# Optimization experiments

Measured on AMD Instinct MI355X. Metric: run time of the kernel, lower is better.

Reference implementation:

```python
import jax, jax.numpy as jnp
import numpy as np

B, D_IMG, D_NUM, P = 16384, 2048, 256, 128

def setup_inputs() -> dict:
    key = jax.random.key(0)
    ks = jax.random.split(key, 12)
    s = lambda d: 1.0 / np.sqrt(d)
    return {
        "img_feat": jax.random.normal(ks[0], (B, D_IMG), jnp.float32),
        "num_feat": jax.random.normal(ks[1], (B, D_NUM), jnp.float32),
        "Wi1": jax.random.uniform(ks[2], (D_IMG, P), jnp.float32, -s(D_IMG), s(D_IMG)),
        "bi1": jax.random.uniform(ks[3], (P,), jnp.float32, -s(D_IMG), s(D_IMG)),
        "Wi2": jax.random.uniform(ks[4], (P, P), jnp.float32, -s(P), s(P)),
        "bi2": jax.random.uniform(ks[5], (P,), jnp.float32, -s(P), s(P)),
        "Wn1": jax.random.uniform(ks[6], (D_NUM, P), jnp.float32, -s(D_NUM), s(D_NUM)),
        "bn1": jax.random.uniform(ks[7], (P,), jnp.float32, -s(D_NUM), s(D_NUM)),
        "Wn2": jax.random.uniform(ks[8], (P, P), jnp.float32, -s(P), s(P)),
        "bn2": jax.random.uniform(ks[9], (P,), jnp.float32, -s(P), s(P)),
        "log_temp": jnp.asarray(np.log(0.1), jnp.float32),
    }

def _mlp(x, W1, b1, W2, b2):
    h = jax.nn.relu(x @ W1 + b1)
    return h @ W2 + b2

def _l2norm(x, eps=1e-12):
    # matches F.normalize(dim=1): x / max(||x||, eps)
    n = jnp.sqrt(jnp.sum(x * x, axis=1, keepdims=True))
    return x / jnp.maximum(n, eps)

def reference(img_feat, num_feat, Wi1, bi1, Wi2, bi2, Wn1, bn1, Wn2, bn2, log_temp):
    temp = jnp.exp(log_temp)
    ip = _l2norm(_mlp(img_feat, Wi1, bi1, Wi2, bi2))  # [B, P]
    npj = _l2norm(_mlp(num_feat, Wn1, bn1, Wn2, bn2))  # [B, P]
    logits = (ip @ npj.T) / temp                        # [B, B]
    # symmetric cross-entropy with labels = arange(B): targets on the diagonal
    lse_rows = jax.nn.logsumexp(logits, axis=1)  # i2n
    lse_cols = jax.nn.logsumexp(logits, axis=0)  # n2i (logits.T rows)
    diag = jnp.diagonal(logits)
    loss_i2n = jnp.mean(lse_rows - diag)
    loss_n2i = jnp.mean(lse_cols - diag)
    return (loss_i2n + loss_n2i) * 0.5
```

## Files before the change

### kernel.cpp

```cpp
#include <hip/hip_runtime.h>
#include <hip/hip_bf16.h>

typedef __bf16 bf16_t;
typedef __bf16 bf16x8 __attribute__((ext_vector_type(8)));
typedef __bf16 bf16x4 __attribute__((ext_vector_type(4)));
typedef float f32x4 __attribute__((ext_vector_type(4)));

#define NB 16384
#define PP 128
#define NSPLIT 16
#define CG (NB / NSPLIT)
#define BNT 64
#define NT (CG / BNT)

__device__ inline bf16x8 ld8(const bf16_t* p) { return *(const bf16x8*)p; }

__device__ inline void gload_lds16(const bf16_t* g, bf16_t* l) {
  __builtin_amdgcn_global_load_lds(
      (const __attribute__((address_space(1))) unsigned int*)g,
      (__attribute__((address_space(3))) unsigned int*)l, 16, 0, 0);
}

__global__ void transpose_all(const float* __restrict__ Wi1, const float* __restrict__ Wn1,
                              const float* __restrict__ Wi2, const float* __restrict__ Wn2,
                              bf16_t* __restrict__ Wi1t, bf16_t* __restrict__ Wn1t,
                              bf16_t* __restrict__ Wi2t, bf16_t* __restrict__ Wn2t) {
  int idx = blockIdx.x * 256 + threadIdx.x;
  if (idx < 2048 * 128) { int k = idx >> 7, n = idx & 127; Wi1t[n * 2048 + k] = (bf16_t)Wi1[idx]; return; }
  idx -= 2048 * 128;
  if (idx < 256 * 128)  { int k = idx >> 7, n = idx & 127; Wn1t[n * 256 + k]  = (bf16_t)Wn1[idx]; return; }
  idx -= 256 * 128;
  if (idx < 128 * 128)  { int k = idx >> 7, n = idx & 127; Wi2t[n * 128 + k]  = (bf16_t)Wi2[idx]; return; }
  idx -= 128 * 128;
  if (idx < 128 * 128)  { int k = idx >> 7, n = idx & 127; Wn2t[n * 128 + k]  = (bf16_t)Wn2[idx]; }
}

__global__ __launch_bounds__(256, 4) void mlp1_combined(
    const float* __restrict__ Ximg, const float* __restrict__ Xnum,
    const bf16_t* __restrict__ Wit, const bf16_t* __restrict__ Wnt,
    const float* __restrict__ bi, const float* __restrict__ bn,
    bf16_t* __restrict__ Himg, bf16_t* __restrict__ Hnum) {
  __shared__ bf16_t As[32 * 128];
  __shared__ bf16_t Bs[128 * 128];
  const int bid = blockIdx.x;
  const bool isnum = bid >= 512;
  const float* X = isnum ? Xnum : Ximg;
  const bf16_t* Wt = isnum ? Wnt : Wit;
  const float* bias = isnum ? bn : bi;
  bf16_t* H = isnum ? Hnum : Himg;
  const int K = isnum ? 256 : 2048;
  const int t = threadIdx.x, l = t & 63, wid = t >> 6;
  const int wm = wid >> 1, wn = wid & 1;
  const int row0 = (bid & 511) * 32;

  f32x4 acc[4];
#pragma unroll
  for (int j = 0; j < 4; j++) acc[j] = (f32x4){0.f, 0.f, 0.f, 0.f};

  for (int k0 = 0; k0 < K; k0 += 128) {
    __syncthreads();
#pragma unroll
    for (int i = 0; i < 4; i++) {
      int s = t + i * 256;
      int r = s >> 5, c4 = s & 31;
      const float4 f = *(const float4*)(X + (size_t)(row0 + r) * K + k0 + c4 * 4);
      bf16x4 pk;
      pk[0] = (bf16_t)f.x; pk[1] = (bf16_t)f.y; pk[2] = (bf16_t)f.z; pk[3] = (bf16_t)f.w;
      int chunk = c4 >> 1, half = c4 & 1;
      *(bf16x4*)(As + r * 128 + ((chunk ^ (r & 7)) << 3) + half * 4) = pk;
    }
#pragma unroll
    for (int i = 0; i < 8; i++) {
      int s = t + i * 256;
      int r = s >> 4, c = s & 15;
      bf16x8 v = ld8(Wt + (size_t)r * K + k0 + c * 8);
      *(bf16x8*)(Bs + r * 128 + ((c ^ (r & 7)) << 3)) = v;
    }
    __syncthreads();
#pragma unroll
    for (int ks = 0; ks < 4; ks++) {
      int r = wm * 16 + (l & 15);
      int c = ks * 4 + (l >> 4);
      bf16x8 a = ld8(As + r * 128 + ((c ^ (r & 7)) << 3));
#pragma unroll
      for (int nt = 0; nt < 4; nt++) {
        int rb = wn * 64 + nt * 16 + (l & 15);
        bf16x8 b = ld8(Bs + rb * 128 + ((c ^ (rb & 7)) << 3));
        acc[nt] = __builtin_amdgcn_mfma_f32_16x16x32_bf16(a, b, acc[nt], 0, 0, 0);
      }
    }
  }
  int rbase = row0 + wm * 16 + ((l >> 4) << 2);
#pragma unroll
  for (int nt = 0; nt < 4; nt++) {
    int col = wn * 64 + nt * 16 + (l & 15);
    float bv = bias[col];
#pragma unroll
    for (int r4 = 0; r4 < 4; r4++) {
      float v = acc[nt][r4] + bv;
      H[(size_t)(rbase + r4) * PP + col] = (bf16_t)fmaxf(v, 0.f);
    }
  }
}

__global__ __launch_bounds__(256, 3) void mlp2_combined(
    const bf16_t* __restrict__ Himg, const bf16_t* __restrict__ Hnum,
    const bf16_t* __restrict__ Wi2t, const bf16_t* __restrict__ Wn2t,
    const float* __restrict__ bi2, const float* __restrict__ bn2,
    bf16_t* __restrict__ OutI, bf16_t* __restrict__ OutN) {
  __shared__ bf16_t As[32 * 128];
  __shared__ bf16_t Bs[128 * 128];
  __shared__ float rnorm[32];
  const int bid = blockIdx.x;
  const bool isnum = bid >= 512;
  const bf16_t* Hin = isnum ? Hnum : Himg;
  const bf16_t* W2t = isnum ? Wn2t : Wi2t;
  const float* bias = isnum ? bn2 : bi2;
  bf16_t* Out = isnum ? OutN : OutI;
  const int t = threadIdx.x, l = t & 63, wid = t >> 6;
  const int wm = wid >> 1, wn = wid & 1;
  const int row0 = (bid & 511) * 32;
  if (t < 32) rnorm[t] = 0.f;
#pragma unroll
  for (int i = 0; i < 2; i++) {
    int s = t + i * 256;
    int r = s >> 4, c = s & 15;
    bf16x8 v = ld8(Hin + (size_t)(row0 + r) * 128 + c * 8);
    *(bf16x8*)(As + r * 128 + ((c ^ (r & 7)) << 3)) = v;
  }
#pragma unroll
  for (int i = 0; i < 8; i++) {
    int s = t + i * 256;
    int r = s >> 4, c = s & 15;
    bf16x8 v = ld8(W2t + (size_t)r * 128 + c * 8);
    *(bf16x8*)(Bs + r * 128 + ((c ^ (r & 7)) << 3)) = v;
  }
  __syncthreads();
  f32x4 acc[4];
#pragma unroll
  for (int j = 0; j < 4; j++) acc[j] = (f32x4){0.f, 0.f, 0.f, 0.f};
#pragma unroll
  for (int ks = 0; ks < 4; ks++) {
    int r = wm * 16 + (l & 15);
    int c = ks * 4 + (l >> 4);
    bf16x8 a = ld8(As + r * 128 + ((c ^ (r & 7)) << 3));
#pragma unroll
    for (int nt = 0; nt < 4; nt++) {
      int rb = wn * 64 + nt * 16 + (l & 15);
      bf16x8 b = ld8(Bs + rb * 128 + ((c ^ (rb & 7)) << 3));
      acc[nt] = __builtin_amdgcn_mfma_f32_16x16x32_bf16(a, b, acc[nt], 0, 0, 0);
    }
  }
  float vv[4][4];
#pragma unroll
  for (int nt = 0; nt < 4; nt++) {
    int col = wn * 64 + nt * 16 + (l & 15);
    float bv = bias[col];
#pragma unroll
    for (int r4 = 0; r4 < 4; r4++) vv[nt][r4] = acc[nt][r4] + bv;
  }
#pragma unroll
  for (int r4 = 0; r4 < 4; r4++) {
    float p = 0.f;
#pragma unroll
    for (int nt = 0; nt < 4; nt++) p += vv[nt][r4] * vv[nt][r4];
    p += __shfl_xor(p, 1); p += __shfl_xor(p, 2);
    p += __shfl_xor(p, 4); p += __shfl_xor(p, 8);
    if ((l & 15) == 0) atomicAdd(&rnorm[wm * 16 + ((l >> 4) << 2) + r4], p);
  }
  __syncthreads();
#pragma unroll
  for (int r4 = 0; r4 < 4; r4++) {
    int rl = wm * 16 + ((l >> 4) << 2) + r4;
    float sc = 1.f / fmaxf(sqrtf(rnorm[rl]), 1e-12f);
#pragma unroll
    for (int nt = 0; nt < 4; nt++) {
      int col = wn * 64 + nt * 16 + (l & 15);
      int swcol = (((col >> 3) ^ (rl & 7)) << 3) | (col & 7);
      Out[(size_t)(row0 + rl) * 128 + swcol] = (bf16_t)(vv[nt][r4] * sc);
    }
  }
}

__global__ __launch_bounds__(256, 3) void logits_split(
    const bf16_t* __restrict__ IP, const bf16_t* __restrict__ NP,
    const float* __restrict__ log_temp, float* __restrict__ rowpart,
    float* __restrict__ colpart, float* __restrict__ diag) {
  __shared__ bf16_t BsAll[2 * BNT * 128];
  __shared__ float colred[2][CG];
  __shared__ float rowred[2][128];
  int bid = blockIdx.x;
  int sw = (bid & 7) * (128 * NSPLIT / 8) + (bid >> 3);
  int bm = sw >> 4, g = sw & (NSPLIT - 1);
  const int t = threadIdx.x, l = t & 63, wid = t >> 6;
  const int wm = wid >> 1, wn = wid & 1;
  const float invt = __expf(-log_temp[0]);
  const float kk = invt * 1.44269504088896f;

#pragma unroll
  for (int i = 0; i < 8; i++) {
    int s = t + i * 256;
    gload_lds16(IP + (size_t)bm * (128 * 128) + s * 8, BsAll + s * 8);
  }
  __syncthreads();
  bf16x8 af[4][4];
#pragma unroll
  for (int mt = 0; mt < 4; mt++) {
    int r = wm * 64 + mt * 16 + (l & 15);
#pragma unroll
    for (int ks = 0; ks < 4; ks++) {
      int c = ks * 4 + (l >> 4);
      af[mt][ks] = ld8(BsAll + r * 128 + ((c ^ (r & 7)) << 3));
    }
  }
  __syncthreads();
#pragma unroll
  for (int i = 0; i < 4; i++) {
    int s = t + i * 256;
    gload_lds16(NP + (size_t)(g * CG) * 128 + s * 8, BsAll + s * 8);
  }
  __syncthreads();

  f32x4 racc[4];
#pragma unroll
  for (int a = 0; a < 4; a++) racc[a] = (f32x4){0.f, 0.f, 0.f, 0.f};

#pragma unroll 1
  for (int tl = 0; tl < NT; tl++) {
    bf16_t* Bsc = BsAll + (tl & 1) * (BNT * 128);
    if (tl + 1 < NT) {
      bf16_t* Bsn = BsAll + ((tl + 1) & 1) * (BNT * 128);
      const bf16_t* src = NP + (size_t)(g * CG + (tl + 1) * BNT) * 128;
#pragma unroll
      for (int i = 0; i < 4; i++) {
        int s = t + i * 256;
        gload_lds16(src + s * 8, Bsn + s * 8);
      }
    }
    f32x4 acc[4][2];
#pragma unroll
    for (int i = 0; i < 4; i++)
#pragma unroll
      for (int j = 0; j < 2; j++) acc[i][j] = (f32x4){0.f, 0.f, 0.f, 0.f};
#pragma unroll
    for (int ks = 0; ks < 4; ks++) {
      int c = ks * 4 + (l >> 4);
      bf16x8 b[2];
#pragma unroll
      for (int nt = 0; nt < 2; nt++) {
        int rb = wn * 32 + nt * 16 + (l & 15);
        b[nt] = ld8(Bsc + rb * 128 + ((c ^ (rb & 7)) << 3));
      }
#pragma unroll
      for (int mt = 0; mt < 4; mt++) {
        acc[mt][0] = __builtin_amdgcn_mfma_f32_16x16x32_bf16(af[mt][ks], b[0], acc[mt][0], 0, 0, 0);
        acc[mt][1] = __builtin_amdgcn_mfma_f32_16x16x32_bf16(af[mt][ks], b[1], acc[mt][1], 0, 0, 0);
      }
    }
    const int colbase = g * CG + tl * BNT;
    if ((colbase >> 7) == bm) {
#pragma unroll
      for (int mt = 0; mt < 4; mt++)
#pragma unroll
        for (int nt = 0; nt < 2; nt++)
#pragma unroll
          for (int r4 = 0; r4 < 4; r4++) {
            int gr = bm * 128 + wm * 64 + mt * 16 + ((l >> 4) << 2) + r4;
            int gc = colbase + wn * 32 + nt * 16 + (l & 15);
            if (gr == gc) diag[gr] = acc[mt][nt][r4] * invt;
          }
    }
#pragma unroll
    for (int mt = 0; mt < 4; mt++)
#pragma unroll
      for (int nt = 0; nt < 2; nt++) {
        f32x4 y = acc[mt][nt] * kk - kk;
#pragma unroll
        for (int r4 = 0; r4 < 4; r4++) acc[mt][nt][r4] = __builtin_amdgcn_exp2f(y[r4]);
      }
#pragma unroll
    for (int mt = 0; mt < 4; mt++) racc[mt] += acc[mt][0] + acc[mt][1];
#pragma unroll
    for (int nt = 0; nt < 2; nt++) {
      f32x4 cv = (acc[0][nt] + acc[1][nt]) + (acc[2][nt] + acc[3][nt]);
      float cs = (cv[0] + cv[1]) + (cv[2] + cv[3]);
      cs += __shfl_xor(cs, 16); cs += __shfl_xor(cs, 32);
      if (l < 16) colred[wm][tl * BNT + wn * 32 + nt * 16 + l] = cs;
    }
    __syncthreads();
  }
#pragma unroll
  for (int mt = 0; mt < 4; mt++)
#pragma unroll
    for (int r4 = 0; r4 < 4; r4++) {
      float rs = racc[mt][r4];
      rs += __shfl_xor(rs, 1); rs += __shfl_xor(rs, 2);
      rs += __shfl_xor(rs, 4); rs += __shfl_xor(rs, 8);
      if ((l & 15) == 0)
        rowred[wn][wm * 64 + mt * 16 + ((l >> 4) << 2) + r4] = rs;
    }
  __syncthreads();
  if (t < 128)
    rowpart[(size_t)g * NB + bm * 128 + t] = rowred[0][t] + rowred[1][t];
  for (int c = t; c < CG; c += 256)
    colpart[(size_t)bm * NB + g * CG + c] = colred[0][c] + colred[1][c];
}

__global__ void finalize1(const float* __restrict__ rowpart, const float* __restrict__ colpart,
                          const float* __restrict__ diag, float* __restrict__ lossacc) {
  int i = blockIdx.x * 64 + threadIdx.x;
  float rsum = 0.f, csum = 0.f;
#pragma unroll
  for (int g = 0; g < NSPLIT; g++) rsum += rowpart[(size_t)g * NB + i];
#pragma unroll 16
  for (int b = 0; b < 128; b++) csum += colpart[(size_t)b * NB + i];
  float v = 0.5f * (logf(rsum) + logf(csum)) - diag[i];
  for (int m = 1; m < 64; m <<= 1) v += __shfl_xor(v, m);
  if (threadIdx.x == 0) atomicAdd(lossacc, v);
}

__global__ void finalize2(const float* __restrict__ lossacc,
                          const float* __restrict__ log_temp, float* __restrict__ out) {
  out[0] = lossacc[0] / (float)NB + __expf(-log_temp[0]);
}

extern "C" void kernel_launch(void* const* d_in, const int* in_sizes, int n_in,
                              void* d_out, int out_size, void* d_ws, size_t ws_size,
                              hipStream_t stream) {
  const float* img = (const float*)d_in[0];
  const float* num = (const float*)d_in[1];
  const float* Wi1 = (const float*)d_in[2];
  const float* bi1 = (const float*)d_in[3];
  const float* Wi2 = (const float*)d_in[4];
  const float* bi2 = (const float*)d_in[5];
  const float* Wn1 = (const float*)d_in[6];
  const float* bn1 = (const float*)d_in[7];
  const float* Wn2 = (const float*)d_in[8];
  const float* bn2 = (const float*)d_in[9];
  const float* log_temp = (const float*)d_in[10];
  float* out = (float*)d_out;

  char* w = (char*)d_ws;
  bf16_t* ipb   = (bf16_t*)(w);
  bf16_t* npb   = (bf16_t*)(w + (4u << 20));
  bf16_t* h_img = (bf16_t*)(w + (8u << 20));
  bf16_t* h_num = (bf16_t*)(w + (12u << 20));
  float*  colpart = (float*)(w + (8u << 20));
  bf16_t* Wi1t  = (bf16_t*)(w + (16u << 20));
  bf16_t* Wn1t  = (bf16_t*)(w + (16u << 20) + (512u << 10));
  bf16_t* Wi2t  = (bf16_t*)(w + (16u << 20) + (576u << 10));
  bf16_t* Wn2t  = (bf16_t*)(w + (16u << 20) + (640u << 10));
  float*  rowpart = (float*)(w + (16u << 20));
  float*  diag  = (float*)(w + (17u << 20));
  float*  lossacc = (float*)(w + (17u << 20) + (64u << 10));

  hipMemsetAsync(lossacc, 0, sizeof(float), stream);

  transpose_all<<<dim3(1280), 256, 0, stream>>>(Wi1, Wn1, Wi2, Wn2, Wi1t, Wn1t, Wi2t, Wn2t);

  mlp1_combined<<<dim3(1024), 256, 0, stream>>>(img, num, Wi1t, Wn1t, bi1, bn1, h_img, h_num);
  mlp2_combined<<<dim3(1024), 256, 0, stream>>>(h_img, h_num, Wi2t, Wn2t, bi2, bn2, ipb, npb);

  logits_split<<<dim3(128 * NSPLIT), 256, 0, stream>>>(ipb, npb, log_temp, rowpart, colpart, diag);
  finalize1<<<dim3(NB / 64), 64, 0, stream>>>(rowpart, colpart, diag, lossacc);
  finalize2<<<dim3(1), 1, 0, stream>>>(lossacc, log_temp, out);
}
```

Measured before the change: 335.1 us.

## Fuse MLP layers, pre-convert inputs to bf16, widen logits blocks, merge finalize

Fuses the two MLP layers into one kernel so the hidden activations stay in LDS instead of going through global memory. When the workspace is large enough, a prep kernel first converts the inputs to swizzled bf16, and the MLP then loads them with direct global-to-LDS copies. The logits kernel moves to 512-thread blocks with fewer row tiles per wave and accumulates column sums with LDS atomics. The two finalize kernels and the memset are merged using a last-block counter. The input pre-conversion adds a full extra pass over the 128MB image input, and the 512-thread blocks change occupancy and register pressure.

```diff
diff --git a/kernel.cpp b/kernel.cpp
--- a/kernel.cpp
+++ b/kernel.cpp
@@ -3,11 +3,9 @@
 
 typedef __bf16 bf16_t;
 typedef __bf16 bf16x8 __attribute__((ext_vector_type(8)));
-typedef __bf16 bf16x4 __attribute__((ext_vector_type(4)));
 typedef float f32x4 __attribute__((ext_vector_type(4)));
 
 #define NB 16384
-#define PP 128
 #define NSPLIT 16
 #define CG (NB / NSPLIT)
 #define BNT 64
@@ -21,124 +19,156 @@
       (__attribute__((address_space(3))) unsigned int*)l, 16, 0, 0);
 }
 
-__global__ void transpose_all(const float* __restrict__ Wi1, const float* __restrict__ Wn1,
-                              const float* __restrict__ Wi2, const float* __restrict__ Wn2,
-                              bf16_t* __restrict__ Wi1t, bf16_t* __restrict__ Wn1t,
-                              bf16_t* __restrict__ Wi2t, bf16_t* __restrict__ Wn2t) {
-  int idx = blockIdx.x * 256 + threadIdx.x;
-  if (idx < 2048 * 128) { int k = idx >> 7, n = idx & 127; Wi1t[n * 2048 + k] = (bf16_t)Wi1[idx]; return; }
-  idx -= 2048 * 128;
-  if (idx < 256 * 128)  { int k = idx >> 7, n = idx & 127; Wn1t[n * 256 + k]  = (bf16_t)Wn1[idx]; return; }
-  idx -= 256 * 128;
-  if (idx < 128 * 128)  { int k = idx >> 7, n = idx & 127; Wi2t[n * 128 + k]  = (bf16_t)Wi2[idx]; return; }
-  idx -= 128 * 128;
-  if (idx < 128 * 128)  { int k = idx >> 7, n = idx & 127; Wn2t[n * 128 + k]  = (bf16_t)Wn2[idx]; }
-}
-
-__global__ __launch_bounds__(256, 4) void mlp1_combined(
-    const float* __restrict__ Ximg, const float* __restrict__ Xnum,
-    const bf16_t* __restrict__ Wit, const bf16_t* __restrict__ Wnt,
-    const float* __restrict__ bi, const float* __restrict__ bn,
-    bf16_t* __restrict__ Himg, bf16_t* __restrict__ Hnum) {
-  __shared__ bf16_t As[32 * 128];
-  __shared__ bf16_t Bs[128 * 128];
-  const int bid = blockIdx.x;
-  const bool isnum = bid >= 512;
-  const float* X = isnum ? Xnum : Ximg;
-  const bf16_t* Wt = isnum ? Wnt : Wit;
-  const float* bias = isnum ? bn : bi;
-  bf16_t* H = isnum ? Hnum : Himg;
-  const int K = isnum ? 256 : 2048;
-  const int t = threadIdx.x, l = t & 63, wid = t >> 6;
-  const int wm = wid >> 1, wn = wid & 1;
-  const int row0 = (bid & 511) * 32;
-
-  f32x4 acc[4];
-#pragma unroll
-  for (int j = 0; j < 4; j++) acc[j] = (f32x4){0.f, 0.f, 0.f, 0.f};
-
-  for (int k0 = 0; k0 < K; k0 += 128) {
-    __syncthreads();
+__global__ void prep(const float* __restrict__ img, const float* __restrict__ num,
+                     const float* __restrict__ Wi1, const float* __restrict__ Wn1,
+                     const float* __restrict__ Wi2, const float* __restrict__ Wn2,
+                     bf16_t* __restrict__ imgb, bf16_t* __restrict__ numb,
+                     bf16_t* __restrict__ Wi1t, bf16_t* __restrict__ Wn1t,
+                     bf16_t* __restrict__ Wi2t, bf16_t* __restrict__ Wn2t,
+                     float* __restrict__ lossacc, int nimg, int nnum) {
+  int b = blockIdx.x;
+  if (b < nimg) {
+    int base = b * 8192;
 #pragma unroll
     for (int i = 0; i < 4; i++) {
-      int s = t + i * 256;
-      int r = s >> 5, c4 = s & 31;
-      const float4 f = *(const float4*)(X + (size_t)(row0 + r) * K + k0 + c4 * 4);
-      bf16x4 pk;
-      pk[0] = (bf16_t)f.x; pk[1] = (bf16_t)f.y; pk[2] = (bf16_t)f.z; pk[3] = (bf16_t)f.w;
-      int chunk = c4 >> 1, half = c4 & 1;
-      *(bf16x4*)(As + r * 128 + ((chunk ^ (r & 7)) << 3) + half * 4) = pk;
-    }
-#pragma unroll
-    for (int i = 0; i < 8; i++) {
-      int s = t + i * 256;
-      int r = s >> 4, c = s & 15;
-      bf16x8 v = ld8(Wt + (size_t)r * K + k0 + c * 8);
-      *(bf16x8*)(Bs + r * 128 + ((c ^ (r & 7)) << 3)) = v;
-    }
-    __syncthreads();
-#pragma unroll
-    for (int ks = 0; ks < 4; ks++) {
-      int r = wm * 16 + (l & 15);
-      int c = ks * 4 + (l >> 4);
-      bf16x8 a = ld8(As + r * 128 + ((c ^ (r & 7)) << 3));
-#pragma unroll
-      for (int nt = 0; nt < 4; nt++) {
-        int rb = wn * 64 + nt * 16 + (l & 15);
-        bf16x8 b = ld8(Bs + rb * 128 + ((c ^ (rb & 7)) << 3));
-        acc[nt] = __builtin_amdgcn_mfma_f32_16x16x32_bf16(a, b, acc[nt], 0, 0, 0);
-      }
-    }
-  }
-  int rbase = row0 + wm * 16 + ((l >> 4) << 2);
-#pragma unroll
-  for (int nt = 0; nt < 4; nt++) {
-    int col = wn * 64 + nt * 16 + (l & 15);
-    float bv = bias[col];
-#pragma unroll
-    for (int r4 = 0; r4 < 4; r4++) {
-      float v = acc[nt][r4] + bv;
-      H[(size_t)(rbase + r4) * PP + col] = (bf16_t)fmaxf(v, 0.f);
-    }
-  }
-}
-
-__global__ __launch_bounds__(256, 3) void mlp2_combined(
-    const bf16_t* __restrict__ Himg, const bf16_t* __restrict__ Hnum,
+      int e = base + (threadIdx.x + i * 256) * 8;
+      int row = e >> 11, k = e & 2047;
+      float4 f0 = *(const float4*)(img + e);
+      float4 f1 = *(const float4*)(img + e + 4);
+      bf16x8 v;
+      v[0]=(bf16_t)f0.x; v[1]=(bf16_t)f0.y; v[2]=(bf16_t)f0.z; v[3]=(bf16_t)f0.w;
+      v[4]=(bf16_t)f1.x; v[5]=(bf16_t)f1.y; v[6]=(bf16_t)f1.z; v[7]=(bf16_t)f1.w;
+      *(bf16x8*)(imgb + (size_t)row * 2048 + (k ^ ((row & 7) << 3))) = v;
+    }
+    return;
+  }
+  b -= nimg;
+  if (b < nnum) {
+    int base = b * 8192;
+#pragma unroll
+    for (int i = 0; i < 4; i++) {
+      int e = base + (threadIdx.x + i * 256) * 8;
+      int row = e >> 8, k = e & 255;
+      float4 f0 = *(const float4*)(num + e);
+      float4 f1 = *(const float4*)(num + e + 4);
+      bf16x8 v;
+      v[0]=(bf16_t)f0.x; v[1]=(bf16_t)f0.y; v[2]=(bf16_t)f0.z; v[3]=(bf16_t)f0.w;
+      v[4]=(bf16_t)f1.x; v[5]=(bf16_t)f1.y; v[6]=(bf16_t)f1.z; v[7]=(bf16_t)f1.w;
+      *(bf16x8*)(numb + (size_t)row * 256 + (k ^ ((row & 7) << 3))) = v;
+    }
+    return;
+  }
+  b -= nnum;
+  if (b < 1280) {
+    int idx = b * 256 + threadIdx.x;
+    if (idx < 262144) { int k = idx >> 7, n = idx & 127;
+      Wi1t[n * 2048 + (k ^ ((n & 7) << 3))] = (bf16_t)Wi1[idx]; return; }
+    idx -= 262144;
+    if (idx < 32768) { int k = idx >> 7, n = idx & 127;
+      Wn1t[n * 256 + (k ^ ((n & 7) << 3))] = (bf16_t)Wn1[idx]; return; }
+    idx -= 32768;
+    if (idx < 16384) { int k = idx >> 7, n = idx & 127;
+      Wi2t[n * 128 + (k ^ ((n & 7) << 3))] = (bf16_t)Wi2[idx]; return; }
+    idx -= 16384;
+    { int k = idx >> 7, n = idx & 127;
+      Wn2t[n * 128 + (k ^ ((n & 7) << 3))] = (bf16_t)Wn2[idx]; }
+  } else {
+    if (threadIdx.x < 2) lossacc[threadIdx.x] = 0.f;
+  }
+}
+
+template <bool PRE>
+__global__ __launch_bounds__(256, 4) void mlp_fused(
+    const bf16_t* __restrict__ imgb, const bf16_t* __restrict__ numb,
+    const float* __restrict__ imgf, const float* __restrict__ numf,
+    const bf16_t* __restrict__ Wi1t, const bf16_t* __restrict__ Wn1t,
     const bf16_t* __restrict__ Wi2t, const bf16_t* __restrict__ Wn2t,
+    const float* __restrict__ bi1, const float* __restrict__ bn1,
     const float* __restrict__ bi2, const float* __restrict__ bn2,
-    bf16_t* __restrict__ OutI, bf16_t* __restrict__ OutN) {
+    bf16_t* __restrict__ ipb, bf16_t* __restrict__ npb) {
   __shared__ bf16_t As[32 * 128];
   __shared__ bf16_t Bs[128 * 128];
   __shared__ float rnorm[32];
   const int bid = blockIdx.x;
   const bool isnum = bid >= 512;
-  const bf16_t* Hin = isnum ? Hnum : Himg;
-  const bf16_t* W2t = isnum ? Wn2t : Wi2t;
-  const float* bias = isnum ? bn2 : bi2;
-  bf16_t* Out = isnum ? OutN : OutI;
+  const bf16_t* Xb = isnum ? numb : imgb;
+  const float*  Xf = isnum ? numf : imgf;
+  const bf16_t* W1 = isnum ? Wn1t : Wi1t;
+  const bf16_t* W2 = isnum ? Wn2t : Wi2t;
+  const float* b1  = isnum ? bn1 : bi1;
+  const float* b2  = isnum ? bn2 : bi2;
+  bf16_t* Out = isnum ? npb : ipb;
+  const int K = isnum ? 256 : 2048;
   const int t = threadIdx.x, l = t & 63, wid = t >> 6;
   const int wm = wid >> 1, wn = wid & 1;
   const int row0 = (bid & 511) * 32;
   if (t < 32) rnorm[t] = 0.f;
-#pragma unroll
-  for (int i = 0; i < 2; i++) {
-    int s = t + i * 256;
-    int r = s >> 4, c = s & 15;
-    bf16x8 v = ld8(Hin + (size_t)(row0 + r) * 128 + c * 8);
-    *(bf16x8*)(As + r * 128 + ((c ^ (r & 7)) << 3)) = v;
+
+  f32x4 acc[4];
+#pragma unroll
+  for (int j = 0; j < 4; j++) acc[j] = (f32x4){0.f, 0.f, 0.f, 0.f};
+
+  for (int k0 = 0; k0 < K; k0 += 128) {
+    __syncthreads();
+#pragma unroll
+    for (int i = 0; i < 2; i++) {
+      int s = t + i * 256;
+      if constexpr (PRE) {
+        gload_lds16(Xb + (size_t)(row0 + (s >> 4)) * K + k0 + (s & 15) * 8, As + s * 8);
+      } else {
+        int r = s >> 4, c = s & 15;
+        const float* src = Xf + (size_t)(row0 + r) * K + k0 + c * 8;
+        float4 f0 = *(const float4*)(src);
+        float4 f1 = *(const float4*)(src + 4);
+        bf16x8 v;
+        v[0]=(bf16_t)f0.x; v[1]=(bf16_t)f0.y; v[2]=(bf16_t)f0.z; v[3]=(bf16_t)f0.w;
+        v[4]=(bf16_t)f1.x; v[5]=(bf16_t)f1.y; v[6]=(bf16_t)f1.z; v[7]=(bf16_t)f1.w;
+        *(bf16x8*)(As + r * 128 + ((c ^ (r & 7)) << 3)) = v;
+      }
+    }
+#pragma unroll
+    for (int i = 0; i < 8; i++) {
+      int s = t + i * 256;
+      gload_lds16(W1 + (size_t)(s >> 4) * K + k0 + (s & 15) * 8, Bs + s * 8);
+    }
+    __syncthreads();
+#pragma unroll
+    for (int ks = 0; ks < 4; ks++) {
+      int r = wm * 16 + (l & 15);
+      int c = ks * 4 + (l >> 4);
+      bf16x8 a = ld8(As + r * 128 + ((c ^ (r & 7)) << 3));
+#pragma unroll
+      for (int nt = 0; nt < 4; nt++) {
+        int rb = wn * 64 + nt * 16 + (l & 15);
+        bf16x8 bfr = ld8(Bs + rb * 128 + ((c ^ (rb & 7)) << 3));
+        acc[nt] = __builtin_amdgcn_mfma_f32_16x16x32_bf16(a, bfr, acc[nt], 0, 0, 0);
+      }
+    }
+  }
+  __syncthreads();
+  {
+    int rbase = wm * 16 + ((l >> 4) << 2);
+#pragma unroll
+    for (int nt = 0; nt < 4; nt++) {
+      int col = wn * 64 + nt * 16 + (l & 15);
+      float bv = b1[col];
+#pragma unroll
+      for (int r4 = 0; r4 < 4; r4++) {
+        int row = rbase + r4;
+        float h = fmaxf(acc[nt][r4] + bv, 0.f);
+        As[row * 128 + (col ^ ((row & 7) << 3))] = (bf16_t)h;
+      }
+    }
   }
 #pragma unroll
   for (int i = 0; i < 8; i++) {
     int s = t + i * 256;
-    int r = s >> 4, c = s & 15;
-    bf16x8 v = ld8(W2t + (size_t)r * 128 + c * 8);
-    *(bf16x8*)(Bs + r * 128 + ((c ^ (r & 7)) << 3)) = v;
-  }
-  __syncthreads();
-  f32x4 acc[4];
-#pragma unroll
-  for (int j = 0; j < 4; j++) acc[j] = (f32x4){0.f, 0.f, 0.f, 0.f};
+    gload_lds16(W2 + (size_t)(s >> 4) * 128 + (s & 15) * 8, Bs + s * 8);
+  }
+  __syncthreads();
+  f32x4 acc2[4];
+#pragma unroll
+  for (int j = 0; j < 4; j++) acc2[j] = (f32x4){0.f, 0.f, 0.f, 0.f};
 #pragma unroll
   for (int ks = 0; ks < 4; ks++) {
     int r = wm * 16 + (l & 15);
@@ -147,17 +177,17 @@
 #pragma unroll
     for (int nt = 0; nt < 4; nt++) {
       int rb = wn * 64 + nt * 16 + (l & 15);
-      bf16x8 b = ld8(Bs + rb * 128 + ((c ^ (rb & 7)) << 3));
-      acc[nt] = __builtin_amdgcn_mfma_f32_16x16x32_bf16(a, b, acc[nt], 0, 0, 0);
+      bf16x8 bfr = ld8(Bs + rb * 128 + ((c ^ (rb & 7)) << 3));
+      acc2[nt] = __builtin_amdgcn_mfma_f32_16x16x32_bf16(a, bfr, acc2[nt], 0, 0, 0);
     }
   }
   float vv[4][4];
 #pragma unroll
   for (int nt = 0; nt < 4; nt++) {
     int col = wn * 64 + nt * 16 + (l & 15);
-    float bv = bias[col];
-#pragma unroll
-    for (int r4 = 0; r4 < 4; r4++) vv[nt][r4] = acc[nt][r4] + bv;
+    float bv = b2[col];
+#pragma unroll
+    for (int r4 = 0; r4 < 4; r4++) vv[nt][r4] = acc2[nt][r4] + bv;
   }
 #pragma unroll
   for (int r4 = 0; r4 < 4; r4++) {
@@ -176,18 +206,18 @@
 #pragma unroll
     for (int nt = 0; nt < 4; nt++) {
       int col = wn * 64 + nt * 16 + (l & 15);
-      int swcol = (((col >> 3) ^ (rl & 7)) << 3) | (col & 7);
+      int swcol = col ^ ((rl & 7) << 3);
       Out[(size_t)(row0 + rl) * 128 + swcol] = (bf16_t)(vv[nt][r4] * sc);
     }
   }
 }
 
-__global__ __launch_bounds__(256, 3) void logits_split(
+__global__ __launch_bounds__(512, 6) void logits_split(
     const bf16_t* __restrict__ IP, const bf16_t* __restrict__ NP,
     const float* __restrict__ log_temp, float* __restrict__ rowpart,
     float* __restrict__ colpart, float* __restrict__ diag) {
   __shared__ bf16_t BsAll[2 * BNT * 128];
-  __shared__ float colred[2][CG];
+  __shared__ float colred[CG];
   __shared__ float rowred[2][128];
   int bid = blockIdx.x;
   int sw = (bid & 7) * (128 * NSPLIT / 8) + (bid >> 3);
@@ -197,16 +227,17 @@
   const float invt = __expf(-log_temp[0]);
   const float kk = invt * 1.44269504088896f;
 
-#pragma unroll
-  for (int i = 0; i < 8; i++) {
-    int s = t + i * 256;
+  for (int i = t; i < CG; i += 512) colred[i] = 0.f;
+#pragma unroll
+  for (int i = 0; i < 4; i++) {
+    int s = t + i * 512;
     gload_lds16(IP + (size_t)bm * (128 * 128) + s * 8, BsAll + s * 8);
   }
   __syncthreads();
-  bf16x8 af[4][4];
-#pragma unroll
-  for (int mt = 0; mt < 4; mt++) {
-    int r = wm * 64 + mt * 16 + (l & 15);
+  bf16x8 af[2][4];
+#pragma unroll
+  for (int mt = 0; mt < 2; mt++) {
+    int r = wm * 32 + mt * 16 + (l & 15);
 #pragma unroll
     for (int ks = 0; ks < 4; ks++) {
       int c = ks * 4 + (l >> 4);
@@ -215,15 +246,15 @@
   }
   __syncthreads();
 #pragma unroll
-  for (int i = 0; i < 4; i++) {
-    int s = t + i * 256;
+  for (int i = 0; i < 2; i++) {
+    int s = t + i * 512;
     gload_lds16(NP + (size_t)(g * CG) * 128 + s * 8, BsAll + s * 8);
   }
   __syncthreads();
 
-  f32x4 racc[4];
-#pragma unroll
-  for (int a = 0; a < 4; a++) racc[a] = (f32x4){0.f, 0.f, 0.f, 0.f};
+  f32x4 racc[2];
+  racc[0] = (f32x4){0.f, 0.f, 0.f, 0.f};
+  racc[1] = (f32x4){0.f, 0.f, 0.f, 0.f};
 
 #pragma unroll 1
   for (int tl = 0; tl < NT; tl++) {
@@ -232,14 +263,14 @@
       bf16_t* Bsn = BsAll + ((tl + 1) & 1) * (BNT * 128);
       const bf16_t* src = NP + (size_t)(g * CG + (tl + 1) * BNT) * 128;
 #pragma unroll
-      for (int i = 0; i < 4; i++) {
-        int s = t + i * 256;
+      for (int i = 0; i < 2; i++) {
+        int s = t + i * 512;
         gload_lds16(src + s * 8, Bsn + s * 8);
       }
     }
-    f32x4 acc[4][2];
-#pragma unroll
-    for (int i = 0; i < 4; i++)
+    f32x4 acc[2][2];
+#pragma unroll
+    for (int i = 0; i < 2; i++)
 #pragma unroll
       for (int j = 0; j < 2; j++) acc[i][j] = (f32x4){0.f, 0.f, 0.f, 0.f};
 #pragma unroll
@@ -252,7 +283,7 @@
         b[nt] = ld8(Bsc + rb * 128 + ((c ^ (rb & 7)) << 3));
       }
 #pragma unroll
-      for (int mt = 0; mt < 4; mt++) {
+      for (int mt = 0; mt < 2; mt++) {
         acc[mt][0] = __builtin_amdgcn_mfma_f32_16x16x32_bf16(af[mt][ks], b[0], acc[mt][0], 0, 0, 0);
         acc[mt][1] = __builtin_amdgcn_mfma_f32_16x16x32_bf16(af[mt][ks], b[1], acc[mt][1], 0, 0, 0);
       }
@@ -260,18 +291,18 @@
     const int colbase = g * CG + tl * BNT;
     if ((colbase >> 7) == bm) {
 #pragma unroll
-      for (int mt = 0; mt < 4; mt++)
+      for (int mt = 0; mt < 2; mt++)
 #pragma unroll
         for (int nt = 0; nt < 2; nt++)
 #pragma unroll
           for (int r4 = 0; r4 < 4; r4++) {
-            int gr = bm * 128 + wm * 64 + mt * 16 + ((l >> 4) << 2) + r4;
+            int gr = bm * 128 + wm * 32 + mt * 16 + ((l >> 4) << 2) + r4;
             int gc = colbase + wn * 32 + nt * 16 + (l & 15);
             if (gr == gc) diag[gr] = acc[mt][nt][r4] * invt;
           }
     }
 #pragma unroll
-    for (int mt = 0; mt < 4; mt++)
+    for (int mt = 0; mt < 2; mt++)
 #pragma unroll
       for (int nt = 0; nt < 2; nt++) {
         f32x4 y = acc[mt][nt] * kk - kk;
@@ -279,35 +310,36 @@
         for (int r4 = 0; r4 < 4; r4++) acc[mt][nt][r4] = __builtin_amdgcn_exp2f(y[r4]);
       }
 #pragma unroll
-    for (int mt = 0; mt < 4; mt++) racc[mt] += acc[mt][0] + acc[mt][1];
+    for (int mt = 0; mt < 2; mt++) racc[mt] += acc[mt][0] + acc[mt][1];
 #pragma unroll
     for (int nt = 0; nt < 2; nt++) {
-      f32x4 cv = (acc[0][nt] + acc[1][nt]) + (acc[2][nt] + acc[3][nt]);
+      f32x4 cv = acc[0][nt] + acc[1][nt];
       float cs = (cv[0] + cv[1]) + (cv[2] + cv[3]);
       cs += __shfl_xor(cs, 16); cs += __shfl_xor(cs, 32);
-      if (l < 16) colred[wm][tl * BNT + wn * 32 + nt * 16 + l] = cs;
+      if (l < 16) atomicAdd(&colred[tl * BNT + wn * 32 + nt * 16 + l], cs);
     }
     __syncthreads();
   }
 #pragma unroll
-  for (int mt = 0; mt < 4; mt++)
+  for (int mt = 0; mt < 2; mt++)
 #pragma unroll
     for (int r4 = 0; r4 < 4; r4++) {
       float rs = racc[mt][r4];
       rs += __shfl_xor(rs, 1); rs += __shfl_xor(rs, 2);
       rs += __shfl_xor(rs, 4); rs += __shfl_xor(rs, 8);
       if ((l & 15) == 0)
-        rowred[wn][wm * 64 + mt * 16 + ((l >> 4) << 2) + r4] = rs;
+        rowred[wn][wm * 32 + mt * 16 + ((l >> 4) << 2) + r4] = rs;
     }
   __syncthreads();
   if (t < 128)
     rowpart[(size_t)g * NB + bm * 128 + t] = rowred[0][t] + rowred[1][t];
-  for (int c = t; c < CG; c += 256)
-    colpart[(size_t)bm * NB + g * CG + c] = colred[0][c] + colred[1][c];
-}
-
-__global__ void finalize1(const float* __restrict__ rowpart, const float* __restrict__ colpart,
-                          const float* __restrict__ diag, float* __restrict__ lossacc) {
+  for (int c = t; c < CG; c += 512)
+    colpart[(size_t)bm * NB + g * CG + c] = colred[c];
+}
+
+__global__ void finalize(const float* __restrict__ rowpart, const float* __restrict__ colpart,
+                         const float* __restrict__ diag, const float* __restrict__ log_temp,
+                         float* __restrict__ lossacc, float* __restrict__ out) {
   int i = blockIdx.x * 64 + threadIdx.x;
   float rsum = 0.f, csum = 0.f;
 #pragma unroll
@@ -316,12 +348,15 @@
   for (int b = 0; b < 128; b++) csum += colpart[(size_t)b * NB + i];
   float v = 0.5f * (logf(rsum) + logf(csum)) - diag[i];
   for (int m = 1; m < 64; m <<= 1) v += __shfl_xor(v, m);
-  if (threadIdx.x == 0) atomicAdd(lossacc, v);
-}
-
-__global__ void finalize2(const float* __restrict__ lossacc,
-                          const float* __restrict__ log_temp, float* __restrict__ out) {
-  out[0] = lossacc[0] / (float)NB + __expf(-log_temp[0]);
+  if (threadIdx.x == 0) {
+    atomicAdd(lossacc, v);
+    __threadfence();
+    unsigned n = atomicAdd((unsigned*)(lossacc + 1), 1u);
+    if (n == gridDim.x - 1) {
+      float tot = atomicAdd(lossacc, 0.f);
+      out[0] = tot / (float)NB + __expf(-log_temp[0]);
+    }
+  }
 }
 
 extern "C" void kernel_launch(void* const* d_in, const int* in_sizes, int n_in,
@@ -341,27 +376,51 @@
   float* out = (float*)d_out;
 
   char* w = (char*)d_ws;
-  bf16_t* ipb   = (bf16_t*)(w);
-  bf16_t* npb   = (bf16_t*)(w + (4u << 20));
-  bf16_t* h_img = (bf16_t*)(w + (8u << 20));
-  bf16_t* h_num = (bf16_t*)(w + (12u << 20));
-  float*  colpart = (float*)(w + (8u << 20));
-  bf16_t* Wi1t  = (bf16_t*)(w + (16u << 20));
-  bf16_t* Wn1t  = (bf16_t*)(w + (16u << 20) + (512u << 10));
-  bf16_t* Wi2t  = (bf16_t*)(w + (16u << 20) + (576u << 10));
-  bf16_t* Wn2t  = (bf16_t*)(w + (16u << 20) + (640u << 10));
-  float*  rowpart = (float*)(w + (16u << 20));
-  float*  diag  = (float*)(w + (17u << 20));
-  float*  lossacc = (float*)(w + (17u << 20) + (64u << 10));
-
-  hipMemsetAsync(lossacc, 0, sizeof(float), stream);
-
-  transpose_all<<<dim3(1280), 256, 0, stream>>>(Wi1, Wn1, Wi2, Wn2, Wi1t, Wn1t, Wi2t, Wn2t);
-
-  mlp1_combined<<<dim3(1024), 256, 0, stream>>>(img, num, Wi1t, Wn1t, bi1, bn1, h_img, h_num);
-  mlp2_combined<<<dim3(1024), 256, 0, stream>>>(h_img, h_num, Wi2t, Wn2t, bi2, bn2, ipb, npb);
-
-  logits_split<<<dim3(128 * NSPLIT), 256, 0, stream>>>(ipb, npb, log_temp, rowpart, colpart, diag);
-  finalize1<<<dim3(NB / 64), 64, 0, stream>>>(rowpart, colpart, diag, lossacc);
-  finalize2<<<dim3(1), 1, 0, stream>>>(lossacc, log_temp, out);
-}
+  bf16_t* ipb  = (bf16_t*)(w);
+  bf16_t* npb  = (bf16_t*)(w + (4u << 20));
+  float* colpart = (float*)(w + (8u << 20));
+
+  const size_t need_big = (90ull << 20) + (64ull << 10) + 8;
+  const bool big = ws_size >= need_big;
+
+  bf16_t *imgb, *numb, *Wi1t, *Wn1t, *Wi2t, *Wn2t;
+  float *rowpart, *diag, *lossacc;
+  if (big) {
+    imgb = (bf16_t*)(w + (16u << 20));
+    numb = (bf16_t*)(w + (80u << 20));
+    Wi1t = (bf16_t*)(w + (88u << 20));
+    Wn1t = (bf16_t*)(w + (88u << 20) + (512u << 10));
+    Wi2t = (bf16_t*)(w + (88u << 20) + (576u << 10));
+    Wn2t = (bf16_t*)(w + (88u << 20) + (640u << 10));
+    rowpart = (float*)(w + (89u << 20));
+    diag    = (float*)(w + (90u << 20));
+    lossacc = (float*)(w + (90u << 20) + (64u << 10));
+  } else {
+    imgb = numb = (bf16_t*)w;
+    Wi1t = (bf16_t*)(w + (16u << 20));
+    Wn1t = (bf16_t*)(w + (16u << 20) + (512u << 10));
+    Wi2t = (bf16_t*)(w + (16u << 20) + (576u << 10));
+    Wn2t = (bf16_t*)(w + (16u << 20) + (640u << 10));
+    rowpart = (float*)(w + (16u << 20));
+    diag    = (float*)(w + (17u << 20));
+    lossacc = (float*)(w + (17u << 20) + (64u << 10));
+  }
+
+  const int nimg = big ? 4096 : 0, nnum = big ? 512 : 0;
+  prep<<<dim3(nimg + nnum + 1280 + 1), 256, 0, stream>>>(
+      img, num, Wi1, Wn1, Wi2, Wn2, imgb, numb, Wi1t, Wn1t, Wi2t, Wn2t,
+      lossacc, nimg, nnum);
+  if (big) {
+    mlp_fused<true><<<dim3(1024), 256, 0, stream>>>(
+        imgb, numb, img, num, Wi1t, Wn1t, Wi2t, Wn2t,
+        bi1, bn1, bi2, bn2, ipb, npb);
+  } else {
+    mlp_fused<false><<<dim3(1024), 256, 0, stream>>>(
+        imgb, numb, img, num, Wi1t, Wn1t, Wi2t, Wn2t,
+        bi1, bn1, bi2, bn2, ipb, npb);
+  }
+  logits_split<<<dim3(128 * NSPLIT), 512, 0, stream>>>(ipb, npb, log_temp,
+                                                       rowpart, colpart, diag);
+  finalize<<<dim3(NB / 64), 64, 0, stream>>>(rowpart, colpart, diag, log_temp,
+                                             lossacc, out);
+}
```

Measured after the change: 412.5 us. 23.1% more time.
